# Kernel optimization log

Measured on AMD Instinct MI355X. Metric: run time of the kernel, lower is better.

Reference implementation:

```python
import jax, jax.numpy as jnp
import numpy as np

N = 100000      # num nodes
T = 4           # num edge types
E = 150000      # edges per edge type
HID = 128       # hidden_dim
NH = 8          # num_heads
D = 16          # per_head_dim
MS = NH * D     # message size


def setup_inputs() -> dict:
    key = jax.random.key(0)
    ks = jax.random.split(key, 6)
    x = jax.random.normal(ks[0], (N, HID), dtype=jnp.float32)
    adj = jax.random.randint(ks[1], (T, E, 2), 0, N, dtype=jnp.int32)
    Wq = jax.random.normal(ks[2], (T, HID, MS), dtype=jnp.float32) * 0.05
    Wk = jax.random.normal(ks[3], (T, HID, MS), dtype=jnp.float32) * 0.05
    Wm = jax.random.normal(ks[4], (T, 2 * HID, MS), dtype=jnp.float32) * 0.05
    bm = jnp.zeros((T, MS), dtype=jnp.float32)
    return {"x": x, "adj": adj, "Wq": Wq, "Wk": Wk, "Wm": Wm, "bm": bm}


def reference(x, adj, Wq, Wk, Wm, bm):
    scale = D ** (-0.5)
    srcs = adj[..., 0]  # [T, E]
    tgts = adj[..., 1]  # [T, E]
    xs = x[srcs]        # [T, E, HID] gather
    xt = x[tgts]        # [T, E, HID] gather
    # per-edge-type message MLP (depth 1 -> single linear + relu)
    feats = jnp.concatenate([xs, xt], axis=-1)                 # [T, E, 2*HID]
    msgs = jax.nn.relu(jnp.einsum('tef,tfm->tem', feats, Wm) + bm[:, None, :])
    msgs = msgs.reshape(T * E, NH, D)
    # per-edge-type Q/K projections and per-head dot-product scores
    q = (scale * jnp.einsum('teh,thm->tem', xt, Wq)).reshape(T * E, NH, D)
    k = jnp.einsum('teh,thm->tem', xs, Wk).reshape(T * E, NH, D)
    scores = jnp.einsum('ehd,ehd->eh', q, k)                   # [T*E, NH]
    idx = tgts.reshape(-1)                                     # [T*E]
    # segment (scatter) softmax over edges grouped by target node
    m = jax.ops.segment_max(scores, idx, num_segments=N)       # [N, NH]
    m = jnp.where(jnp.isfinite(m), m, jnp.zeros_like(m))       # empty segments
    e = jnp.exp(scores - m[idx])
    denom = jax.ops.segment_sum(e, idx, num_segments=N)        # [N, NH]
    probs = e / denom[idx]                                     # [T*E, NH]
    # weighted scatter-sum aggregation
    agg = jax.ops.segment_sum(probs[..., None] * msgs, idx, num_segments=N)
    return agg.reshape(N, MS)
```

## Files before the change

kernel.cpp:

```cpp
#include <hip/hip_runtime.h>
#include <hip/hip_bf16.h>
#include <cstdint>

#define NND 100000
#define NT 4
#define NE 150000
#define TOTE (NT * NE)
#define HID 128
#define NHD 8
#define MS 128
#define SEL ((size_t)NND * MS)
#define BAT 8
#define PNW 32

typedef __bf16 bf16x8 __attribute__((ext_vector_type(8)));
typedef float f32x4 __attribute__((ext_vector_type(4)));
typedef unsigned int u32x4 __attribute__((ext_vector_type(4)));

__device__ __forceinline__ float bf2f(unsigned int u16) {
  unsigned int b = u16 << 16;
  return __builtin_bit_cast(float, b);
}
__device__ __forceinline__ unsigned short f2bf(float f) {
  unsigned int b = __builtin_bit_cast(unsigned int, f);
  b += 0x7FFFu + ((b >> 16) & 1u);
  return (unsigned short)(b >> 16);
}

__global__ void k_convert_x(const float* __restrict__ x, unsigned short* __restrict__ xb) {
  int i = (blockIdx.x * 256 + threadIdx.x) * 4;
  float4 v = *reinterpret_cast<const float4*>(x + i);
  ushort4 o;
  o.x = f2bf(v.x); o.y = f2bf(v.y); o.z = f2bf(v.z); o.w = f2bf(v.w);
  *reinterpret_cast<ushort4*>(xb + i) = o;
}

__global__ void k_pack_w(const float* __restrict__ Wq, const float* __restrict__ Wk,
                         const float* __restrict__ Wm, unsigned short* __restrict__ wp) {
  int p = blockIdx.x * 256 + threadIdx.x;
  int e    = p & 7;
  int lane = (p >> 3) & 63;
  int b    = (p >> 9) & 3;
  int c    = (p >> 11) & 7;
  int kind = (p >> 14) & 3;
  int t    = p >> 16;
  int col = c * 16 + (lane & 15);
  int k   = b * 32 + (lane >> 4) * 8 + e;
  float v;
  if (kind == 0)      v = 0.25f * Wq[((size_t)t * HID + k) * MS + col];
  else if (kind == 1) v = Wk[((size_t)t * HID + k) * MS + col];
  else if (kind == 2) v = Wm[((size_t)t * 2 * HID + k) * MS + col];
  else                v = Wm[((size_t)t * 2 * HID + HID + k) * MS + col];
  wp[p] = f2bf(v);
}

__global__ void k_hist(const int* __restrict__ adj, int* __restrict__ counts, int tshift) {
  int i = blockIdx.x * 256 + threadIdx.x;
  if (i < TOTE) {
    int win = (i / NE) >> tshift;
    atomicAdd(&counts[win * NND + adj[2 * i + 1]], 1);
  }
}

__global__ void k_blocksum(const int* __restrict__ counts, int* __restrict__ bsum, int ntot) {
  __shared__ int s[4];
  int i = blockIdx.x * 256 + threadIdx.x;
  int v = (i < ntot) ? counts[i] : 0;
#pragma unroll
  for (int d = 1; d < 64; d <<= 1) v += __shfl_xor(v, d);
  if ((threadIdx.x & 63) == 0) s[threadIdx.x >> 6] = v;
  __syncthreads();
  if (threadIdx.x == 0) bsum[blockIdx.x] = s[0] + s[1] + s[2] + s[3];
}

__global__ void k_scan_mid(int* __restrict__ bsum, int nb, int* __restrict__ offsets,
                           int ntot) {
  __shared__ int s[1024];
  int t = threadIdx.x;
  s[t] = (t < nb) ? bsum[t] : 0;
  __syncthreads();
  for (int d = 1; d < 1024; d <<= 1) {
    int u = (t >= d) ? s[t - d] : 0;
    __syncthreads();
    s[t] += u;
    __syncthreads();
  }
  if (t < nb) bsum[t] = (t > 0) ? s[t - 1] : 0;
  if (t == 0) offsets[ntot] = TOTE;
}

__global__ void k_scan_add(const int* __restrict__ counts, const int* __restrict__ bsum,
                           int* __restrict__ offsets, int* __restrict__ cursor, int ntot) {
  __shared__ int s[256];
  int b = blockIdx.x, t = threadIdx.x, i = b * 256 + t;
  s[t] = (i < ntot) ? counts[i] : 0;
  __syncthreads();
  for (int d = 1; d < 256; d <<= 1) {
    int u = (t >= d) ? s[t - d] : 0;
    __syncthreads();
    s[t] += u;
    __syncthreads();
  }
  int excl = ((t > 0) ? s[t - 1] : 0) + bsum[b];
  if (i < ntot) { offsets[i] = excl; cursor[i] = excl; }
}

__global__ void k_scatter(const int* __restrict__ adj, int* __restrict__ cursor,
                          int* __restrict__ edata, int tshift) {
  int i = blockIdx.x * 256 + threadIdx.x;
  if (i >= TOTE) return;
  int src = adj[2 * i], tgt = adj[2 * i + 1];
  int t = i / NE;
  int win = t >> tshift;
  int rel = t & ((1 << tshift) - 1);
  int pos = atomicAdd(&cursor[win * NND + tgt], 1);
  edata[pos] = (rel << 24) | (rel * NND + src);
}

__global__ __launch_bounds__(256) void k_projF(const unsigned short* __restrict__ xb,
                                               const unsigned short* __restrict__ wp,
                                               const float* __restrict__ bm,
                                               unsigned short* __restrict__ bQ,
                                               unsigned short* __restrict__ bK,
                                               unsigned short* __restrict__ bMs,
                                               unsigned short* __restrict__ bMt,
                                               int tlo, int npass, int cpx) {
  __shared__ unsigned short wlds[16384];
  int flat = blockIdx.x;
  int xcd = flat & 7;
  int idx = flat >> 3;
  int chunk = xcd * cpx + idx / npass;
  int pass  = idx - (idx / npass) * npass;
  if (chunk * 128 >= NND) return;
  int tt = pass >> 2, kind = pass & 3;
  int wave = threadIdx.x >> 6;
  int lane = threadIdx.x & 63;
  int la = lane & 15, kg = lane >> 4;
  int nodeBase = chunk * 128 + wave * PNW;

  {
    const char* gsrc = (const char*)(wp + (size_t)((tlo + tt) * 4 + kind) * 16384) +
                       wave * 8192 + lane * 16;
    char* ldst = (char*)wlds + wave * 8192;
#pragma unroll
    for (int i = 0; i < 8; i++) {
      __builtin_amdgcn_global_load_lds(
          (const __attribute__((address_space(1))) unsigned int*)(gsrc + i * 1024),
          (__attribute__((address_space(3))) unsigned int*)(ldst + i * 1024), 16, 0, 0);
    }
  }

  bf16x8 xf[2][4];
#pragma unroll
  for (int g = 0; g < 2; g++) {
    int node = nodeBase + g * 16 + la;
    if (node < NND) {
      const unsigned short* ap = xb + (size_t)node * HID + kg * 8;
#pragma unroll
      for (int b = 0; b < 4; b++)
        xf[g][b] = *reinterpret_cast<const bf16x8*>(ap + b * 32);
    } else {
#pragma unroll
      for (int b = 0; b < 4; b++)
#pragma unroll
        for (int e = 0; e < 8; e++) xf[g][b][e] = (__bf16)0.0f;
    }
  }

  asm volatile("s_waitcnt vmcnt(0)");
  __syncthreads();

  f32x4 acc[2][8];
#pragma unroll
  for (int g = 0; g < 2; g++)
#pragma unroll
    for (int c = 0; c < 8; c++)
#pragma unroll
      for (int r = 0; r < 4; r++) acc[g][c][r] = 0.0f;

#pragma unroll
  for (int c = 0; c < 8; c++)
#pragma unroll
    for (int b = 0; b < 4; b++) {
      bf16x8 wf = *reinterpret_cast<const bf16x8*>(wlds + (c * 4 + b) * 512 + lane * 8);
      acc[0][c] = __builtin_amdgcn_mfma_f32_16x16x32_bf16(wf, xf[0][b], acc[0][c], 0, 0, 0);
      acc[1][c] = __builtin_amdgcn_mfma_f32_16x16x32_bf16(wf, xf[1][b], acc[1][c], 0, 0, 0);
    }

  __syncthreads();

  unsigned short* ob =
      (kind == 0 ? bQ : kind == 1 ? bK : kind == 2 ? bMs : bMt) + (size_t)tt * SEL;
  const float* bmrow = bm + (size_t)(tlo + tt) * MS;
  bool addb = (kind == 3);
#pragma unroll
  for (int g = 0; g < 2; g++) {
    char* rowp = (char*)wlds + (size_t)(wave * 32 + g * 16 + la) * 256;
    int sw = (la & 7) << 5;
#pragma unroll
    for (int c = 0; c < 8; c++) {
      float b0 = 0.f, b1 = 0.f, b2 = 0.f, b3 = 0.f;
      if (addb) {
        float4 bb = *reinterpret_cast<const float4*>(bmrow + c * 16 + kg * 4);
        b0 = bb.x; b1 = bb.y; b2 = bb.z; b3 = bb.w;
      }
      uint2 o;
      o.x = (unsigned int)f2bf(acc[g][c][0] + b0) |
            ((unsigned int)f2bf(acc[g][c][1] + b1) << 16);
      o.y = (unsigned int)f2bf(acc[g][c][2] + b2) |
            ((unsigned int)f2bf(acc[g][c][3] + b3) << 16);
      *reinterpret_cast<uint2*>(rowp + ((c * 32 + kg * 8) ^ sw)) = o;
    }
  }
#pragma unroll
  for (int p = 0; p < 8; p++) {
    int nidx = p * 4 + kg;
    int node = nodeBase + nidx;
    char* rp = (char*)wlds + (size_t)(wave * 32 + nidx) * 256;
    u32x4 v = *reinterpret_cast<u32x4*>(rp + ((la * 16) ^ ((nidx & 7) << 5)));
    if (node < NND)
      __builtin_nontemporal_store(
          v, reinterpret_cast<u32x4*>(ob + (size_t)node * MS + la * 8));
  }
}

template <int NTP>
__global__ __launch_bounds__(256) void k_edge(const int* __restrict__ edata,
                                              const int* __restrict__ offs,
                                              const unsigned short* __restrict__ qall,
                                              const unsigned short* __restrict__ kall,
                                              const unsigned short* __restrict__ msall,
                                              const unsigned short* __restrict__ mtall,
                                              float* __restrict__ out,
                                              float* __restrict__ denom,
                                              int init, int fin) {
  int wave = threadIdx.x >> 6, lane = threadIdx.x & 63;
  int n = blockIdx.x * 4 + wave;
  if (n >= NND) return;
  int beg = __builtin_amdgcn_readfirstlane(offs[n]);
  int end = __builtin_amdgcn_readfirstlane(offs[n + 1]);
  int h = lane >> 3;

  float dsum = 0.0f, m0 = 0.0f, m1 = 0.0f;

  if (beg < end) {
    unsigned int qv[NTP], mtv[NTP];
#pragma unroll
    for (int tt = 0; tt < NTP; tt++) {
      qv[tt]  = *reinterpret_cast<const unsigned int*>(qall  + ((size_t)tt * NND + n) * MS + lane * 2);
      mtv[tt] = *reinterpret_cast<const unsigned int*>(mtall + ((size_t)tt * NND + n) * MS + lane * 2);
    }

    for (int base = beg; base < end; base += BAT) {
      int ed[BAT];
      unsigned int ku[BAT], mu[BAT];
#pragma unroll
      for (int j = 0; j < BAT; j++) {
        int p = base + j;
        ed[j] = (p < end) ? __builtin_amdgcn_readfirstlane(edata[p]) : -1;
      }
#pragma unroll
      for (int j = 0; j < BAT; j++) {
        if (ed[j] >= 0) {
          int row = ed[j] & 0xFFFFFF;
          ku[j] = *reinterpret_cast<const unsigned int*>(kall  + (size_t)row * MS + lane * 2);
          mu[j] = *reinterpret_cast<const unsigned int*>(msall + (size_t)row * MS + lane * 2);
        }
      }
#pragma unroll
      for (int j = 0; j < BAT; j++) {
        if (ed[j] >= 0) {
          int rel = ed[j] >> 24;
          unsigned int qu, mtu;
          if constexpr (NTP == 2) {
            qu  = rel ? qv[1] : qv[0];
            mtu = rel ? mtv[1] : mtv[0];
          } else {
            qu  = rel == 0 ? qv[0] : rel == 1 ? qv[1] : rel == 2 ? qv[2] : qv[3];
            mtu = rel == 0 ? mtv[0] : rel == 1 ? mtv[1] : rel == 2 ? mtv[2] : mtv[3];
          }
          float part = bf2f(qu & 0xFFFFu) * bf2f(ku[j] & 0xFFFFu) +
                       bf2f(qu >> 16) * bf2f(ku[j] >> 16);
          part += __shfl_xor(part, 1);
          part += __shfl_xor(part, 2);
          part += __shfl_xor(part, 4);
          float ev = __expf(part);
          dsum += ev;
          float a0 = bf2f(mu[j] & 0xFFFFu) + bf2f(mtu & 0xFFFFu);
          float a1 = bf2f(mu[j] >> 16) + bf2f(mtu >> 16);
          m0 += ev * fmaxf(a0, 0.f);
          m1 += ev * fmaxf(a1, 0.f);
        }
      }
    }
  }

  float* op = out + (size_t)n * MS + lane * 2;
  if (!init) {
    float2 prev = *reinterpret_cast<float2*>(op);
    m0 += prev.x; m1 += prev.y;
    dsum += denom[n * NHD + h];
  }
  if (fin) {
    float inv = dsum > 0.f ? 1.0f / dsum : 0.0f;
    float2 o; o.x = m0 * inv; o.y = m1 * inv;
    *reinterpret_cast<float2*>(op) = o;
  } else {
    float2 o; o.x = m0; o.y = m1;
    *reinterpret_cast<float2*>(op) = o;
    if ((lane & 7) == 0) denom[n * NHD + h] = dsum;
  }
}

extern "C" void kernel_launch(void* const* d_in, const int* in_sizes, int n_in,
                              void* d_out, int out_size, void* d_ws, size_t ws_size,
                              hipStream_t stream) {
  const float* x  = (const float*)d_in[0];
  const int* adj  = (const int*)d_in[1];
  const float* Wq = (const float*)d_in[2];
  const float* Wk = (const float*)d_in[3];
  const float* Wm = (const float*)d_in[4];
  const float* bm = (const float*)d_in[5];
  float* out = (float*)d_out;

  char* ws = (char*)d_ws;
  size_t off = 0;
  auto alloc = [&](size_t bytes) -> char* {
    char* p = ws + off;
    off += (bytes + 255) & ~(size_t)255;
    return p;
  };
  unsigned short* xb = (unsigned short*)alloc((size_t)NND * HID * 2);
  unsigned short* wp = (unsigned short*)alloc((size_t)NT * 4 * HID * MS * 2);
  int* counts   = (int*)alloc((size_t)2 * NND * 4);
  int* offsets  = (int*)alloc((size_t)(2 * NND + 1) * 4);
  int* cursor   = (int*)alloc((size_t)2 * NND * 4);
  int* bsum     = (int*)alloc(1024 * 4);
  int* edata    = (int*)alloc((size_t)TOTE * 4);
  float* denom  = (float*)alloc((size_t)NND * NHD * 4);

  size_t avail = (ws_size > off) ? (ws_size - off) : 0;
  const size_t perType = 4 * SEL * 2;
  int TPH = (avail >= 4 * perType) ? 4 : 2;
  int tshift = (TPH == 4) ? 2 : 1;
  int NWIN = NT / TPH;
  int ntot = NWIN * NND;
  unsigned short* region = (unsigned short*)(ws + off);
  unsigned short* bufQ  = region;
  unsigned short* bufK  = region + (size_t)TPH * SEL;
  unsigned short* bufMs = region + (size_t)2 * TPH * SEL;
  unsigned short* bufMt = region + (size_t)3 * TPH * SEL;

  hipMemsetAsync(counts, 0, (size_t)ntot * 4, stream);

  k_convert_x<<<(NND * HID) / (256 * 4), 256, 0, stream>>>(x, xb);
  k_pack_w<<<(NT * 4 * HID * MS) / 256, 256, 0, stream>>>(Wq, Wk, Wm, wp);

  const int NBS = (ntot + 255) / 256;
  k_hist<<<(TOTE + 255) / 256, 256, 0, stream>>>(adj, counts, tshift);
  k_blocksum<<<NBS, 256, 0, stream>>>(counts, bsum, ntot);
  k_scan_mid<<<1, 1024, 0, stream>>>(bsum, NBS, offsets, ntot);
  k_scan_add<<<NBS, 256, 0, stream>>>(counts, bsum, offsets, cursor, ntot);
  k_scatter<<<(TOTE + 255) / 256, 256, 0, stream>>>(adj, cursor, edata, tshift);

  const int nchunks = (NND + 127) / 128;
  const int cpx = (nchunks + 7) / 8;
  const int ngrid = (NND + 3) / 4;

  for (int w = 0; w < NWIN; w++) {
    int tlo = w * TPH;
    int npass = TPH * 4;
    int pgrid = 8 * cpx * npass;
    k_projF<<<pgrid, 256, 0, stream>>>(xb, wp, bm, bufQ, bufK, bufMs, bufMt,
                                       tlo, npass, cpx);
    if (TPH == 2)
      k_edge<2><<<ngrid, 256, 0, stream>>>(edata, offsets + (size_t)w * NND,
                                           bufQ, bufK, bufMs, bufMt, out, denom,
                                           w == 0 ? 1 : 0, (w == NWIN - 1) ? 1 : 0);
    else
      k_edge<4><<<ngrid, 256, 0, stream>>>(edata, offsets + (size_t)w * NND,
                                           bufQ, bufK, bufMs, bufMt, out, denom,
                                           w == 0 ? 1 : 0, (w == NWIN - 1) ? 1 : 0);
  }
}
```

Measured before the change: 328.8 us.

## Fuse x bf16 conversion into projection and process four nodes per edge wave

Drops the separate fp32-to-bf16 conversion kernel and the xb buffer; the projection kernel now reads fp32 x directly and converts in registers. The edge kernel now gives each wave four consecutive target nodes and walks their combined edge range in one batched loop, using per-edge boundary compares to route contributions to four accumulators. This is meant to remove a launch and an intermediate round trip, and to raise the number of edge loads in flight per wave when nodes have few edges. In exchange, each projection block reads twice as many x bytes, and the edge kernel uses more registers and adds branching.

```diff
diff --git a/kernel.cpp b/kernel.cpp
--- a/kernel.cpp
+++ b/kernel.cpp
@@ -25,14 +25,6 @@
   unsigned int b = __builtin_bit_cast(unsigned int, f);
   b += 0x7FFFu + ((b >> 16) & 1u);
   return (unsigned short)(b >> 16);
-}
-
-__global__ void k_convert_x(const float* __restrict__ x, unsigned short* __restrict__ xb) {
-  int i = (blockIdx.x * 256 + threadIdx.x) * 4;
-  float4 v = *reinterpret_cast<const float4*>(x + i);
-  ushort4 o;
-  o.x = f2bf(v.x); o.y = f2bf(v.y); o.z = f2bf(v.z); o.w = f2bf(v.w);
-  *reinterpret_cast<ushort4*>(xb + i) = o;
 }
 
 __global__ void k_pack_w(const float* __restrict__ Wq, const float* __restrict__ Wk,
@@ -117,7 +109,7 @@
   edata[pos] = (rel << 24) | (rel * NND + src);
 }
 
-__global__ __launch_bounds__(256) void k_projF(const unsigned short* __restrict__ xb,
+__global__ __launch_bounds__(256) void k_projF(const float* __restrict__ x,
                                                const unsigned short* __restrict__ wp,
                                                const float* __restrict__ bm,
                                                unsigned short* __restrict__ bQ,
@@ -155,10 +147,16 @@
   for (int g = 0; g < 2; g++) {
     int node = nodeBase + g * 16 + la;
     if (node < NND) {
-      const unsigned short* ap = xb + (size_t)node * HID + kg * 8;
-#pragma unroll
-      for (int b = 0; b < 4; b++)
-        xf[g][b] = *reinterpret_cast<const bf16x8*>(ap + b * 32);
+      const float* xp = x + (size_t)node * HID + kg * 8;
+#pragma unroll
+      for (int b = 0; b < 4; b++) {
+        float4 v0 = *reinterpret_cast<const float4*>(xp + b * 32);
+        float4 v1 = *reinterpret_cast<const float4*>(xp + b * 32 + 4);
+        bf16x8 f;
+        f[0] = (__bf16)v0.x; f[1] = (__bf16)v0.y; f[2] = (__bf16)v0.z; f[3] = (__bf16)v0.w;
+        f[4] = (__bf16)v1.x; f[5] = (__bf16)v1.y; f[6] = (__bf16)v1.z; f[7] = (__bf16)v1.w;
+        xf[g][b] = f;
+      }
     } else {
 #pragma unroll
       for (int b = 0; b < 4; b++)
@@ -235,21 +233,30 @@
                                               float* __restrict__ denom,
                                               int init, int fin) {
   int wave = threadIdx.x >> 6, lane = threadIdx.x & 63;
-  int n = blockIdx.x * 4 + wave;
-  if (n >= NND) return;
-  int beg = __builtin_amdgcn_readfirstlane(offs[n]);
-  int end = __builtin_amdgcn_readfirstlane(offs[n + 1]);
+  int n0 = (blockIdx.x * 4 + wave) * 4;
+  if (n0 >= NND) return;
+  int beg = __builtin_amdgcn_readfirstlane(offs[n0]);
+  int m1  = __builtin_amdgcn_readfirstlane(offs[n0 + 1]);
+  int m2  = __builtin_amdgcn_readfirstlane(offs[n0 + 2]);
+  int m3  = __builtin_amdgcn_readfirstlane(offs[n0 + 3]);
+  int end = __builtin_amdgcn_readfirstlane(offs[n0 + 4]);
   int h = lane >> 3;
 
-  float dsum = 0.0f, m0 = 0.0f, m1 = 0.0f;
+  float ds[4] = {0.f, 0.f, 0.f, 0.f};
+  float ma[4] = {0.f, 0.f, 0.f, 0.f};
+  float mb[4] = {0.f, 0.f, 0.f, 0.f};
 
   if (beg < end) {
-    unsigned int qv[NTP], mtv[NTP];
-#pragma unroll
-    for (int tt = 0; tt < NTP; tt++) {
-      qv[tt]  = *reinterpret_cast<const unsigned int*>(qall  + ((size_t)tt * NND + n) * MS + lane * 2);
-      mtv[tt] = *reinterpret_cast<const unsigned int*>(mtall + ((size_t)tt * NND + n) * MS + lane * 2);
-    }
+    unsigned int qv[4][NTP], mt[4][NTP];
+#pragma unroll
+    for (int v = 0; v < 4; v++)
+#pragma unroll
+      for (int tt = 0; tt < NTP; tt++) {
+        qv[v][tt] = *reinterpret_cast<const unsigned int*>(
+            qall + ((size_t)tt * NND + n0 + v) * MS + lane * 2);
+        mt[v][tt] = *reinterpret_cast<const unsigned int*>(
+            mtall + ((size_t)tt * NND + n0 + v) * MS + lane * 2);
+      }
 
     for (int base = beg; base < end; base += BAT) {
       int ed[BAT];
@@ -271,13 +278,28 @@
       for (int j = 0; j < BAT; j++) {
         if (ed[j] >= 0) {
           int rel = ed[j] >> 24;
+          int p = base + j;
           unsigned int qu, mtu;
-          if constexpr (NTP == 2) {
-            qu  = rel ? qv[1] : qv[0];
-            mtu = rel ? mtv[1] : mtv[0];
+          if (p < m2) {
+            if (p < m1) {
+              if constexpr (NTP == 2) { qu = rel ? qv[0][1] : qv[0][0]; mtu = rel ? mt[0][1] : mt[0][0]; }
+              else { qu = rel==0?qv[0][0]:rel==1?qv[0][1]:rel==2?qv[0][2]:qv[0][3];
+                     mtu = rel==0?mt[0][0]:rel==1?mt[0][1]:rel==2?mt[0][2]:mt[0][3]; }
+            } else {
+              if constexpr (NTP == 2) { qu = rel ? qv[1][1] : qv[1][0]; mtu = rel ? mt[1][1] : mt[1][0]; }
+              else { qu = rel==0?qv[1][0]:rel==1?qv[1][1]:rel==2?qv[1][2]:qv[1][3];
+                     mtu = rel==0?mt[1][0]:rel==1?mt[1][1]:rel==2?mt[1][2]:mt[1][3]; }
+            }
           } else {
-            qu  = rel == 0 ? qv[0] : rel == 1 ? qv[1] : rel == 2 ? qv[2] : qv[3];
-            mtu = rel == 0 ? mtv[0] : rel == 1 ? mtv[1] : rel == 2 ? mtv[2] : mtv[3];
+            if (p < m3) {
+              if constexpr (NTP == 2) { qu = rel ? qv[2][1] : qv[2][0]; mtu = rel ? mt[2][1] : mt[2][0]; }
+              else { qu = rel==0?qv[2][0]:rel==1?qv[2][1]:rel==2?qv[2][2]:qv[2][3];
+                     mtu = rel==0?mt[2][0]:rel==1?mt[2][1]:rel==2?mt[2][2]:mt[2][3]; }
+            } else {
+              if constexpr (NTP == 2) { qu = rel ? qv[3][1] : qv[3][0]; mtu = rel ? mt[3][1] : mt[3][0]; }
+              else { qu = rel==0?qv[3][0]:rel==1?qv[3][1]:rel==2?qv[3][2]:qv[3][3];
+                     mtu = rel==0?mt[3][0]:rel==1?mt[3][1]:rel==2?mt[3][2]:mt[3][3]; }
+            }
           }
           float part = bf2f(qu & 0xFFFFu) * bf2f(ku[j] & 0xFFFFu) +
                        bf2f(qu >> 16) * bf2f(ku[j] >> 16);
@@ -285,30 +307,41 @@
           part += __shfl_xor(part, 2);
           part += __shfl_xor(part, 4);
           float ev = __expf(part);
-          dsum += ev;
           float a0 = bf2f(mu[j] & 0xFFFFu) + bf2f(mtu & 0xFFFFu);
           float a1 = bf2f(mu[j] >> 16) + bf2f(mtu >> 16);
-          m0 += ev * fmaxf(a0, 0.f);
-          m1 += ev * fmaxf(a1, 0.f);
+          float w0 = ev * fmaxf(a0, 0.f);
+          float w1 = ev * fmaxf(a1, 0.f);
+          if (p < m2) {
+            if (p < m1) { ds[0] += ev; ma[0] += w0; mb[0] += w1; }
+            else        { ds[1] += ev; ma[1] += w0; mb[1] += w1; }
+          } else {
+            if (p < m3) { ds[2] += ev; ma[2] += w0; mb[2] += w1; }
+            else        { ds[3] += ev; ma[3] += w0; mb[3] += w1; }
+          }
         }
       }
     }
   }
 
-  float* op = out + (size_t)n * MS + lane * 2;
-  if (!init) {
-    float2 prev = *reinterpret_cast<float2*>(op);
-    m0 += prev.x; m1 += prev.y;
-    dsum += denom[n * NHD + h];
-  }
-  if (fin) {
-    float inv = dsum > 0.f ? 1.0f / dsum : 0.0f;
-    float2 o; o.x = m0 * inv; o.y = m1 * inv;
-    *reinterpret_cast<float2*>(op) = o;
-  } else {
-    float2 o; o.x = m0; o.y = m1;
-    *reinterpret_cast<float2*>(op) = o;
-    if ((lane & 7) == 0) denom[n * NHD + h] = dsum;
+#pragma unroll
+  for (int v = 0; v < 4; v++) {
+    int n = n0 + v;
+    float dsum = ds[v], m0 = ma[v], m1v = mb[v];
+    float* op = out + (size_t)n * MS + lane * 2;
+    if (!init) {
+      float2 prev = *reinterpret_cast<float2*>(op);
+      m0 += prev.x; m1v += prev.y;
+      dsum += denom[n * NHD + h];
+    }
+    if (fin) {
+      float inv = dsum > 0.f ? 1.0f / dsum : 0.0f;
+      float2 o; o.x = m0 * inv; o.y = m1v * inv;
+      *reinterpret_cast<float2*>(op) = o;
+    } else {
+      float2 o; o.x = m0; o.y = m1v;
+      *reinterpret_cast<float2*>(op) = o;
+      if ((lane & 7) == 0) denom[n * NHD + h] = dsum;
+    }
   }
 }
 
@@ -330,7 +363,6 @@
     off += (bytes + 255) & ~(size_t)255;
     return p;
   };
-  unsigned short* xb = (unsigned short*)alloc((size_t)NND * HID * 2);
   unsigned short* wp = (unsigned short*)alloc((size_t)NT * 4 * HID * MS * 2);
   int* counts   = (int*)alloc((size_t)2 * NND * 4);
   int* offsets  = (int*)alloc((size_t)(2 * NND + 1) * 4);
@@ -353,7 +385,6 @@
 
   hipMemsetAsync(counts, 0, (size_t)ntot * 4, stream);
 
-  k_convert_x<<<(NND * HID) / (256 * 4), 256, 0, stream>>>(x, xb);
   k_pack_w<<<(NT * 4 * HID * MS) / 256, 256, 0, stream>>>(Wq, Wk, Wm, wp);
 
   const int NBS = (ntot + 255) / 256;
@@ -365,21 +396,21 @@
 
   const int nchunks = (NND + 127) / 128;
   const int cpx = (nchunks + 7) / 8;
-  const int ngrid = (NND + 3) / 4;
+  const int ngrid4 = (NND / 4 + 3) / 4;
 
   for (int w = 0; w < NWIN; w++) {
     int tlo = w * TPH;
     int npass = TPH * 4;
     int pgrid = 8 * cpx * npass;
-    k_projF<<<pgrid, 256, 0, stream>>>(xb, wp, bm, bufQ, bufK, bufMs, bufMt,
+    k_projF<<<pgrid, 256, 0, stream>>>(x, wp, bm, bufQ, bufK, bufMs, bufMt,
                                        tlo, npass, cpx);
     if (TPH == 2)
-      k_edge<2><<<ngrid, 256, 0, stream>>>(edata, offsets + (size_t)w * NND,
-                                           bufQ, bufK, bufMs, bufMt, out, denom,
-                                           w == 0 ? 1 : 0, (w == NWIN - 1) ? 1 : 0);
+      k_edge<2><<<ngrid4, 256, 0, stream>>>(edata, offsets + (size_t)w * NND,
+                                            bufQ, bufK, bufMs, bufMt, out, denom,
+                                            w == 0 ? 1 : 0, (w == NWIN - 1) ? 1 : 0);
     else
-      k_edge<4><<<ngrid, 256, 0, stream>>>(edata, offsets + (size_t)w * NND,
-                                           bufQ, bufK, bufMs, bufMt, out, denom,
-                                           w == 0 ? 1 : 0, (w == NWIN - 1) ? 1 : 0);
-  }
-}
+      k_edge<4><<<ngrid4, 256, 0, stream>>>(edata, offsets + (size_t)w * NND,
+                                            bufQ, bufK, bufMs, bufMt, out, denom,
+                                            w == 0 ? 1 : 0, (w == NWIN - 1) ? 1 : 0);
+  }
+}
```

Measured after the change: 372.9 us. +13.4%, slower.
